# Performance work log

Hardware: AMD Instinct MI355X
Metric: run time of the kernel (lower is better)

Reference implementation:

```python
import jax, jax.numpy as jnp
import numpy as np

N, IN, WS, OUT, H = 50000, 256, 128, 32, 4
E, M, K = 800000, 2, 10
D = OUT * H  # 128
NEG_SLOPE = 0.2


def _decay(n, alpha=1.5):
    k = np.arange(1, n + 1)
    x = 1.0 / np.power(k, alpha)
    return (x / x.sum()).astype(np.float32)


def setup_inputs() -> dict:
    key = jax.random.key(0)
    ks = jax.random.split(key, 16)
    h = jax.random.normal(ks[0], (N, IN), dtype=jnp.float32)
    src0 = jax.random.randint(ks[1], (E,), 0, N, dtype=jnp.int32)
    dst0 = jax.random.randint(ks[2], (E,), 0, N, dtype=jnp.int32)
    src1 = jax.random.randint(ks[3], (E,), 0, N, dtype=jnp.int32)
    dst1 = jax.random.randint(ks[4], (E,), 0, N, dtype=jnp.int32)
    s = 0.05
    Wh = jax.random.normal(ks[5], (WS, IN), dtype=jnp.float32) * s
    # layer 0 (per metapath): fc (H*F, WS), attn_l/attn_r (H, F)
    fc0 = jax.random.normal(ks[6], (M, H * OUT, WS), dtype=jnp.float32) * s
    al0 = jax.random.normal(ks[7], (M, H, OUT), dtype=jnp.float32) * s
    ar0 = jax.random.normal(ks[8], (M, H, OUT), dtype=jnp.float32) * s
    # layer 1 (per metapath): fc (H*F, H*F)
    fc1 = jax.random.normal(ks[9], (M, H * OUT, H * OUT), dtype=jnp.float32) * s
    al1 = jax.random.normal(ks[10], (M, H, OUT), dtype=jnp.float32) * s
    ar1 = jax.random.normal(ks[11], (M, H, OUT), dtype=jnp.float32) * s
    Wp1 = jax.random.normal(ks[12], (128, D), dtype=jnp.float32) * s
    bp1 = jnp.zeros((128,), dtype=jnp.float32)
    Wp2 = jax.random.normal(ks[13], (1, 128), dtype=jnp.float32) * s
    return dict(h=h, src0=src0, dst0=dst0, src1=src1, dst1=dst1, Wh=Wh,
                fc0=fc0, al0=al0, ar0=ar0, fc1=fc1, al1=al1, ar1=ar1,
                Wp1=Wp1, bp1=bp1, Wp2=Wp2)


def gat_layer(x, src, dst, fcW, attn_l, attn_r):
    # x: (N, Din); fcW: (H*F, Din)
    ft = (x @ fcW.T).reshape(N, H, OUT)            # (N, H, F)
    el = jnp.sum(ft * attn_l, axis=-1)             # (N, H)
    er = jnp.sum(ft * attn_r, axis=-1)             # (N, H)
    e = jax.nn.leaky_relu(el[src] + er[dst], NEG_SLOPE)  # (E, H)
    # edge softmax over incoming edges of each destination node
    mx = jax.ops.segment_max(e, dst, num_segments=N)     # (N, H)
    ee = jnp.exp(e - mx[dst])
    sm = jax.ops.segment_sum(ee, dst, num_segments=N)    # (N, H)
    a = ee / sm[dst]                                     # (E, H)
    # global top-k over the edge dimension (th.topk dim=0), per head
    scores, idx = jax.lax.top_k(a.T, K)                  # (H, K)
    scores = jax.nn.softmax(scores, axis=-1)             # softmax over k
    a_new = jnp.zeros_like(a).at[idx, jnp.arange(H)[:, None]].set(scores)
    msg = ft[src] * a_new[:, :, None]                    # (E, H, F)
    out = jax.ops.segment_sum(msg, dst, num_segments=N)  # (N, H, F)
    return jax.nn.elu(out).reshape(N, H * OUT)


def reference(h, src0, dst0, src1, dst1, Wh, fc0, al0, ar0, fc1, al1, ar1, Wp1, bp1, Wp2):
    c = _decay(2, 1.5)
    wh = h @ Wh.T  # (N, WS)
    srcs = (src0, src1)
    dsts = (dst0, dst1)
    embs = []
    for i in range(M):
        a = gat_layer(wh, srcs[i], dsts[i], fc0[i], al0[i], ar0[i])  # (N, D)
        b = gat_layer(a, srcs[i], dsts[i], fc1[i], al1[i], ar1[i])   # (N, D)
        embs.append(a * c[0] + b * c[1])
    z = jnp.stack(embs, axis=1)                                      # (N, M, D)
    w = jnp.tanh(z @ Wp1.T + bp1) @ Wp2.T                            # (N, M, 1)
    beta = jax.nn.softmax(w, axis=1)
    return jnp.sum(beta * z, axis=1)                                 # (N, D)
```

## Files before the change

### kernel.cpp

```cpp
#include <hip/hip_runtime.h>
#include <math.h>

#define NN   50000
#define IN_F 256
#define OUTF 32
#define NH   4
#define NE   800000
#define NM   2
#define NK   10
#define ND   128

#define WROWS 32
#define WCK  32

#define NCB  782
#define CCAP 1280
#define DSH  6
#define DMSK 63
#define NSL  32
#define SLW  245

__device__ __forceinline__ float lrelu(float x){ return x >= 0.f ? x : 0.2f*x; }
__device__ __forceinline__ unsigned fmap(float f){
  unsigned u = __float_as_uint(f);
  return (u & 0x80000000u) ? ~u : (u | 0x80000000u);
}
__device__ __forceinline__ float funmap(unsigned u){
  return (u & 0x80000000u) ? __uint_as_float(u & 0x7FFFFFFFu) : __uint_as_float(~u);
}

__global__ __launch_bounds__(256) void k_plpr(
    const float* __restrict__ fc0, const float* __restrict__ al0, const float* __restrict__ ar0,
    const float* __restrict__ fc1, const float* __restrict__ al1, const float* __restrict__ ar1,
    float* __restrict__ plpr)
{
  int idx = blockIdx.x*256 + threadIdx.x;
  if (idx >= 4096) return;
  int w  = idx & 127;
  int hh = (idx >> 7) & 3;
  int lr = (idx >> 9) & 1;
  int m  = (idx >> 10) & 1;
  int L  = (idx >> 11) & 1;
  const float* fc = L ? fc1 : fc0;
  const float* at = L ? (lr ? ar1 : al1) : (lr ? ar0 : al0);
  float s = 0.f;
  for (int f = 0; f < OUTF; f++)
    s += at[(m*NH + hh)*OUTF + f] * fc[((size_t)m*128 + hh*OUTF + f)*128 + w];
  plpr[idx] = s;
}

__global__ __launch_bounds__(256) void k_wh(
    const float* __restrict__ hmat, const float* __restrict__ Whm,
    const float* __restrict__ plpr,
    float* __restrict__ wh, float* __restrict__ el0, float* __restrict__ er0)
{
  __shared__ float hsT[WCK][WROWS + 4];
  __shared__ float wT[WCK][128 + 4];
  __shared__ float PL[16][132];
  const int tid = threadIdx.x;
  const int r0 = blockIdx.x * WROWS;
  const int cgrp = tid & 31;
  const int rgrp = tid >> 5;
  float acc[4][4];
#pragma unroll
  for (int i = 0; i < 4; i++)
#pragma unroll
    for (int j = 0; j < 4; j++) acc[i][j] = 0.f;

  for (int kc = 0; kc < IN_F; kc += WCK){
    {
      int row = tid >> 3, f4 = tid & 7;
      int grow = r0 + row;
      float4 v = make_float4(0.f,0.f,0.f,0.f);
      if (grow < NN) v = *(const float4*)&hmat[(size_t)grow*IN_F + kc + f4*4];
      hsT[f4*4+0][row] = v.x;
      hsT[f4*4+1][row] = v.y;
      hsT[f4*4+2][row] = v.z;
      hsT[f4*4+3][row] = v.w;
    }
#pragma unroll
    for (int it = 0; it < 4; it++){
      int item = it*256 + tid;
      int col = item >> 3, f4 = item & 7;
      float4 v = *(const float4*)&Whm[(size_t)col*IN_F + kc + f4*4];
      wT[f4*4+0][col] = v.x;
      wT[f4*4+1][col] = v.y;
      wT[f4*4+2][col] = v.z;
      wT[f4*4+3][col] = v.w;
    }
    __syncthreads();
    for (int kk = 0; kk < WCK; kk++){
      float4 a = *(const float4*)&hsT[kk][rgrp*4];
      float4 b = *(const float4*)&wT[kk][cgrp*4];
      acc[0][0] += a.x*b.x; acc[0][1] += a.x*b.y; acc[0][2] += a.x*b.z; acc[0][3] += a.x*b.w;
      acc[1][0] += a.y*b.x; acc[1][1] += a.y*b.y; acc[1][2] += a.y*b.z; acc[1][3] += a.y*b.w;
      acc[2][0] += a.z*b.x; acc[2][1] += a.z*b.y; acc[2][2] += a.z*b.z; acc[2][3] += a.z*b.w;
      acc[3][0] += a.w*b.x; acc[3][1] += a.w*b.y; acc[3][2] += a.w*b.z; acc[3][3] += a.w*b.w;
    }
    __syncthreads();
  }
#pragma unroll
  for (int i = 0; i < 4; i++){
    int row = r0 + rgrp*4 + i;
    if (row < NN){
      float4 v = make_float4(acc[i][0], acc[i][1], acc[i][2], acc[i][3]);
      *(float4*)&wh[(size_t)row*ND + cgrp*4] = v;
    }
  }
#pragma unroll
  for (int i = 0; i < 4; i++)
    *(float4*)&wT[rgrp*4 + i][cgrp*4] = make_float4(acc[i][0], acc[i][1], acc[i][2], acc[i][3]);
  for (int i = tid; i < 16*128; i += 256) PL[i >> 7][i & 127] = plpr[i];
  __syncthreads();
  if (tid < 128){
    int r = tid >> 2, tcol = tid & 3;
    int row = r0 + r;
    if (row < NN){
      float a0 = 0.f, a1 = 0.f, a2 = 0.f, a3 = 0.f;
      const float* p0 = &PL[tcol*4+0][0];
      const float* p1 = &PL[tcol*4+1][0];
      const float* p2 = &PL[tcol*4+2][0];
      const float* p3 = &PL[tcol*4+3][0];
      for (int w4 = 0; w4 < 32; w4++){
        float4 v = *(const float4*)&wT[r][w4*4];
        const float4 q0 = *(const float4*)&p0[w4*4];
        const float4 q1 = *(const float4*)&p1[w4*4];
        const float4 q2 = *(const float4*)&p2[w4*4];
        const float4 q3 = *(const float4*)&p3[w4*4];
        a0 += v.x*q0.x; a0 += v.y*q0.y; a0 += v.z*q0.z; a0 += v.w*q0.w;
        a1 += v.x*q1.x; a1 += v.y*q1.y; a1 += v.z*q1.z; a1 += v.w*q1.w;
        a2 += v.x*q2.x; a2 += v.y*q2.y; a2 += v.z*q2.z; a2 += v.w*q2.w;
        a3 += v.x*q3.x; a3 += v.y*q3.y; a3 += v.z*q3.z; a3 += v.w*q3.w;
      }
      int m = tcol >> 1;
      float* dp = (tcol & 1) ? er0 : el0;
      float4 res = make_float4(a0, a1, a2, a3);
      *(float4*)&dp[((size_t)m*NN + row)*4] = res;
    }
  }
}

__global__ __launch_bounds__(256) void k_part(
    const int* __restrict__ s0, const int* __restrict__ d0,
    const int* __restrict__ s1, const int* __restrict__ d1,
    unsigned* __restrict__ ccnt, unsigned long long* __restrict__ coarse)
{
  int m = blockIdx.y;
  const int* sp = m ? s1 : s0;
  const int* dp = m ? d1 : d0;
  __shared__ unsigned hist[NCB], base[NCB], cur[NCB];
  int tid = threadIdx.x;
  for (int j = tid; j < NCB; j += 256){ hist[j] = 0u; cur[j] = 0u; }
  __syncthreads();
  int per = (NE + gridDim.x - 1) / gridDim.x;
  int e0 = blockIdx.x * per;
  int e1 = e0 + per; if (e1 > NE) e1 = NE;
  for (int i = e0 + tid; i < e1; i += 256)
    atomicAdd(&hist[dp[i] >> DSH], 1u);
  __syncthreads();
  for (int j = tid; j < NCB; j += 256)
    base[j] = hist[j] ? atomicAdd(&ccnt[m*NCB + j], hist[j]) : 0u;
  __syncthreads();
  for (int i = e0 + tid; i < e1; i += 256){
    int d = dp[i];
    int b = d >> DSH;
    unsigned loc = atomicAdd(&cur[b], 1u);
    unsigned pos = base[b] + loc;
    if (pos < CCAP)
      coarse[((size_t)m*NCB + b)*CCAP + pos] =
          ((unsigned long long)(unsigned)i << 24)
        | ((unsigned long long)(unsigned)(d & DMSK) << 16)
        | (unsigned long long)(unsigned)sp[i];
  }
}

__global__ __launch_bounds__(256) void k_fused(
    const unsigned* __restrict__ ccnt, const unsigned long long* __restrict__ coarse,
    const float* __restrict__ el, const float* __restrict__ er,
    unsigned long long* __restrict__ cand)
{
  int bb = blockIdx.x, m = blockIdx.y;
  const unsigned long long* ce = coarse + ((size_t)m*NCB + bb)*CCAP;
  unsigned cnt = ccnt[m*NCB + bb]; if (cnt > CCAP) cnt = CCAP;
  const float* elp = el + (size_t)m*NN*4;
  const float* erp = er + (size_t)m*NN*4;
  int tid = threadIdx.x;
  int h = tid & 3, es = tid >> 2;
  int dbase = bb << DSH;

  __shared__ float4 erL[64];
  __shared__ unsigned mxL[64][4];
  __shared__ unsigned long long smL[64][4];
  __shared__ unsigned metaL[CCAP];
  __shared__ unsigned long long smem_u64[CCAP*2];
  float* eL = (float*)smem_u64;
  unsigned long long (*cs)[NK] = (unsigned long long(*)[NK])smem_u64;

  if (tid < 64){
    int d = dbase + tid;
    erL[tid] = (d < NN) ? *(const float4*)&erp[(size_t)d*4] : make_float4(0.f,0.f,0.f,0.f);
  }
  { int j = tid; mxL[j>>2][j&3] = 0u; smL[j>>2][j&3] = 0ULL; }
  __syncthreads();

  {
    unsigned p = es;
    for (; p + 192 < cnt; p += 256){
      unsigned long long v0 = ce[p], v1 = ce[p+64], v2 = ce[p+128], v3 = ce[p+192];
      float g0 = elp[(unsigned)(v0 & 0xFFFFULL)*4 + h];
      float g1 = elp[(unsigned)(v1 & 0xFFFFULL)*4 + h];
      float g2 = elp[(unsigned)(v2 & 0xFFFFULL)*4 + h];
      float g3 = elp[(unsigned)(v3 & 0xFFFFULL)*4 + h];
      unsigned d0 = (unsigned)((v0 >> 16) & 0xFFULL);
      unsigned d1 = (unsigned)((v1 >> 16) & 0xFFULL);
      unsigned d2 = (unsigned)((v2 >> 16) & 0xFFULL);
      unsigned d3 = (unsigned)((v3 >> 16) & 0xFFULL);
      float e0 = lrelu(g0 + ((const float*)&erL[d0])[h]);
      float e1 = lrelu(g1 + ((const float*)&erL[d1])[h]);
      float e2 = lrelu(g2 + ((const float*)&erL[d2])[h]);
      float e3 = lrelu(g3 + ((const float*)&erL[d3])[h]);
      eL[p*4 + h] = e0; eL[(p+64)*4 + h] = e1;
      eL[(p+128)*4 + h] = e2; eL[(p+192)*4 + h] = e3;
      if (h == 0){
        metaL[p]     = ((unsigned)(v0 >> 24) << 8) | d0;
        metaL[p+64]  = ((unsigned)(v1 >> 24) << 8) | d1;
        metaL[p+128] = ((unsigned)(v2 >> 24) << 8) | d2;
        metaL[p+192] = ((unsigned)(v3 >> 24) << 8) | d3;
      }
      atomicMax(&mxL[d0][h], fmap(e0));
      atomicMax(&mxL[d1][h], fmap(e1));
      atomicMax(&mxL[d2][h], fmap(e2));
      atomicMax(&mxL[d3][h], fmap(e3));
    }
    for (; p < cnt; p += 64){
      unsigned long long v = ce[p];
      unsigned src  = (unsigned)(v & 0xFFFFULL);
      unsigned dloc = (unsigned)((v >> 16) & 0xFFULL);
      float e = lrelu(elp[src*4 + h] + ((const float*)&erL[dloc])[h]);
      eL[p*4 + h] = e;
      if (h == 0) metaL[p] = ((unsigned)(v >> 24) << 8) | dloc;
      atomicMax(&mxL[dloc][h], fmap(e));
    }
  }
  __syncthreads();

  for (unsigned p = es; p < cnt; p += 64){
    unsigned dloc = metaL[p] & 255u;
    float e = eL[p*4 + h];
    atomicAdd(&smL[dloc][h],
        (unsigned long long)llrint((double)expf(e - funmap(mxL[dloc][h])) * 1073741824.0));
  }
  __syncthreads();

  unsigned long long top[NK];
#pragma unroll
  for (int k = 0; k < NK; k++) top[k] = 0ULL;
  for (unsigned p = es; p < cnt; p += 64){
    unsigned mt = metaL[p];
    unsigned dloc = mt & 255u;
    unsigned eid  = mt >> 8;
    float e = eL[p*4 + h];
    float smv = (float)((double)smL[dloc][h] * (1.0/1073741824.0));
    float av = expf(e - funmap(mxL[dloc][h])) / smv;
    unsigned long long key = ((unsigned long long)__float_as_uint(av) << 32)
                           | (unsigned long long)(~eid);
    if (key > top[NK-1]){
#pragma unroll
      for (int k = 0; k < NK; k++){
        unsigned long long hi = key > top[k] ? key : top[k];
        unsigned long long lo = key > top[k] ? top[k] : key;
        top[k] = hi; key = lo;
      }
    }
  }
  __syncthreads();

  int row = h*64 + es;
#pragma unroll
  for (int k = 0; k < NK; k++) cs[row][k] = top[k];
  __syncthreads();
  int w = tid >> 6, lane = tid & 63;
  unsigned long long mytop[NK];
#pragma unroll
  for (int k = 0; k < NK; k++) mytop[k] = cs[w*64 + lane][k];
  unsigned long long best = 0ULL; int bp = -1;
#pragma unroll
  for (int k = 0; k < NK; k++) if (mytop[k] > best){ best = mytop[k]; bp = k; }
  for (int r = 0; r < NK; r++){
    unsigned long long b = best; int srcl = lane;
#pragma unroll
    for (int off = 32; off > 0; off >>= 1){
      unsigned long long ob = __shfl_down(b, off, 64);
      int os = __shfl_down(srcl, off, 64);
      if (ob > b){ b = ob; srcl = os; }
    }
    b = __shfl(b, 0, 64); srcl = __shfl(srcl, 0, 64);
    if (lane == 0) cand[(((size_t)m*NH + w)*NCB + blockIdx.x)*NK + r] = b;
    if (lane == srcl && bp >= 0){
#pragma unroll
      for (int k = 0; k < NK; k++) if (k == bp) mytop[k] = 0ULL;
      best = 0ULL; bp = -1;
#pragma unroll
      for (int k = 0; k < NK; k++) if (mytop[k] > best){ best = mytop[k]; bp = k; }
    }
  }
}

__global__ __launch_bounds__(256) void k_merge1(
    const unsigned long long* __restrict__ cand,
    unsigned long long* __restrict__ cand2)
{
  int hh = blockIdx.x, m = blockIdx.y, z = blockIdx.z;
  int tid = threadIdx.x;
  const unsigned long long* cp = cand + ((size_t)m*NH + hh)*((size_t)NCB*NK);
  int start = z*SLW;
  int end = start + SLW; if (end > NCB*NK) end = NCB*NK;
  unsigned long long mykey = (start + tid < end) ? cp[start + tid] : 0ULL;

  __shared__ unsigned long long red[256];
  __shared__ int redpos[256];
  for (int r = 0; r < NK; r++){
    red[tid] = mykey; redpos[tid] = tid;
    __syncthreads();
    for (int st = 128; st > 0; st >>= 1){
      if (tid < st && red[tid+st] > red[tid]){ red[tid] = red[tid+st]; redpos[tid] = redpos[tid+st]; }
      __syncthreads();
    }
    if (tid == 0)
      cand2[(((size_t)m*NH + hh)*NSL + z)*NK + r] = red[0];
    int winner = redpos[0];
    __syncthreads();
    if (tid == winner) mykey = 0ULL;
  }
}

__global__ __launch_bounds__(256) void k_sel(
    const unsigned long long* __restrict__ cand2,
    const int* __restrict__ s0, const int* __restrict__ d0,
    const int* __restrict__ s1, const int* __restrict__ d1,
    const float* __restrict__ ftsrc,
    const int* __restrict__ idsA,
    const float* __restrict__ fcW,
    const float* __restrict__ plpr1,
    int* __restrict__ idsOut, float* __restrict__ valsOut,
    float* __restrict__ el2, float* __restrict__ er2, int layer)
{
  int m = blockIdx.x;
  int tid = threadIdx.x;
  const int* sp = m ? s1 : s0;
  const int* dp = m ? d1 : d0;
  int wv = tid >> 6, lane = tid & 63;

  __shared__ unsigned long long selL[NH][NK];
  __shared__ float scL[NH][NK];
  __shared__ int snL[NH][NK], dL[NH][NK];
  __shared__ int slotOf[NH][NK], srcOf[NH][NK];

  {
    const unsigned long long* cp = cand2 + ((size_t)m*NH + wv)*((size_t)NSL*NK);
    unsigned long long top[NK];
#pragma unroll
    for (int k = 0; k < NK; k++) top[k] = 0ULL;
    for (int i = lane; i < NSL*NK; i += 64){
      unsigned long long key = cp[i];
      if (key > top[NK-1]){
#pragma unroll
        for (int k = 0; k < NK; k++){
          unsigned long long hi = key > top[k] ? key : top[k];
          unsigned long long lo = key > top[k] ? top[k] : key;
          top[k] = hi; key = lo;
        }
      }
    }
    unsigned long long best = 0ULL; int bp = -1;
#pragma unroll
    for (int k = 0; k < NK; k++) if (top[k] > best){ best = top[k]; bp = k; }
    for (int r = 0; r < NK; r++){
      unsigned long long b = best; int srcl = lane;
#pragma unroll
      for (int off = 32; off > 0; off >>= 1){
        unsigned long long ob = __shfl_down(b, off, 64);
        int os = __shfl_down(srcl, off, 64);
        if (ob > b){ b = ob; srcl = os; }
      }
      b = __shfl(b, 0, 64); srcl = __shfl(srcl, 0, 64);
      if (lane == 0) selL[wv][r] = b;
      if (lane == srcl && bp >= 0){
#pragma unroll
        for (int k = 0; k < NK; k++) if (k == bp) top[k] = 0ULL;
        best = 0ULL; bp = -1;
#pragma unroll
        for (int k = 0; k < NK; k++) if (top[k] > best){ best = top[k]; bp = k; }
      }
    }
  }
  __syncthreads();

  if (tid < NH*NK){
    int h = tid / NK, k = tid % NK;
    int e = (int)(~(unsigned)(selL[h][k] & 0xFFFFFFFFULL));
    snL[h][k] = sp[e];
    dL[h][k]  = dp[e];
  }
  __syncthreads();

  if (tid < NH){
    float v0 = __uint_as_float((unsigned)(selL[tid][0] >> 32));
    float p[NK]; float sum = 0.f;
#pragma unroll
    for (int k = 0; k < NK; k++){
      float v = __uint_as_float((unsigned)(selL[tid][k] >> 32));
      p[k] = expf(v - v0); sum += p[k];
    }
#pragma unroll
    for (int k = 0; k < NK; k++) scL[tid][k] = p[k] / sum;
  }

  if (wv == 0){
    int myA = -1;
    if (layer) myA = idsA[m*64 + lane];
    int myid = -1;
    int cnt = 0;
    for (int h = 0; h < NH; h++){
      for (int k = 0; k < NK; k++){
        int sn = snL[h][k], d = dL[h][k];
        int srcslot = sn;
        bool ok = true;
        if (layer){
          unsigned long long mb = __ballot(myA == sn);
          if (mb) srcslot = __ffsll(mb) - 1;
          else ok = false;
        }
        int slot = -1;
        if (ok){
          unsigned long long mm = __ballot(lane < cnt && myid == d);
          if (mm) slot = __ffsll(mm) - 1;
          else { slot = cnt; if (lane == cnt) myid = d; cnt++; }
        }
        if (lane == 0){ slotOf[h][k] = slot; srcOf[h][k] = srcslot; }
      }
    }
    idsOut[m*64 + lane] = (lane < cnt) ? myid : -1;
  }
  __syncthreads();

  float* vals = valsOut + (size_t)m*64*128;
  {
    int h = wv, f = lane;
    if (f < OUTF){
      const float* wr = fcW + ((size_t)m*128 + h*OUTF + f)*128;
      for (int k = 0; k < NK; k++){
        int slot = slotOf[h][k];
        if (slot < 0) continue;
        int srcS = srcOf[h][k];
        const float* x = layer ? (ftsrc + ((size_t)m*64 + srcS)*128)
                               : (ftsrc + (size_t)srcS*128);
        float dsum = 0.f;
        for (int w = 0; w < 128; w++) dsum += x[w] * wr[w];
        vals[(size_t)slot*128 + h*OUTF + f] += scL[h][k] * dsum;
      }
    }
  }
  __syncthreads();

  for (int t = tid; t < 64*128; t += 256){
    int slot = t >> 7, c = t & 127;
    float x = vals[(size_t)slot*128 + c];
    vals[(size_t)slot*128 + c] = x > 0.f ? x : expm1f(x);
  }
  __syncthreads();

  if (layer == 0){
    for (int t = tid; t < 64*8; t += 256){
      int slot = t >> 3, q = t & 7;
      int d = idsOut[m*64 + slot];
      if (d < 0) continue;
      int lr = q >> 2, hh = q & 3;
      const float* P = plpr1 + (((size_t)m*2 + lr)*NH + hh)*128;
      const float* row = vals + (size_t)slot*128;
      float s = 0.f;
      for (int w = 0; w < 128; w++) s += row[w] * P[w];
      float* dpp = lr ? er2 : el2;
      dpp[((size_t)m*NN + d)*4 + hh] = s;
    }
  }
}

__global__ __launch_bounds__(128) void k_final(
    const int* __restrict__ ids, const float* __restrict__ vals,
    const float* __restrict__ Wp1, const float* __restrict__ bp1, const float* __restrict__ Wp2,
    float c0, float c1, float* __restrict__ out)
{
  int j = blockIdx.x;
  int n = ids[j];
  if (n < 0) return;
  for (int q = 0; q < j; q++) if (ids[q] == n) return;
  int tid = threadIdx.x;
  __shared__ float z[2][128];
  __shared__ int slots[4];
  if (tid < 4){
    int sl = -1;
    const int* base = ids + tid*64;
    for (int q = 0; q < 64; q++) if (base[q] == n){ sl = q; break; }
    slots[tid] = sl;
  }
  __syncthreads();
#pragma unroll
  for (int m = 0; m < 2; m++){
    int sa = slots[m], sb = slots[2 + m];
    float av = sa >= 0 ? vals[((size_t)m*64 + sa)*128 + tid] : 0.f;
    float bv = sb >= 0 ? vals[((size_t)(2 + m)*64 + sb)*128 + tid] : 0.f;
    z[m][tid] = c0*av + c1*bv;
  }
  __syncthreads();
  float a0 = bp1[tid], a1 = a0;
  const float* wr = Wp1 + (size_t)tid*128;
  for (int w = 0; w < 128; w++){
    float wv = wr[w];
    a0 += z[0][w]*wv;
    a1 += z[1][w]*wv;
  }
  float t0 = tanhf(a0), t1 = tanhf(a1);
  float w2v = Wp2[tid];
  __shared__ float r0[128], r1[128];
  r0[tid] = t0*w2v; r1[tid] = t1*w2v;
  __syncthreads();
  for (int st = 64; st > 0; st >>= 1){
    if (tid < st){ r0[tid] += r0[tid+st]; r1[tid] += r1[tid+st]; }
    __syncthreads();
  }
  __shared__ float b0s, b1s;
  if (tid == 0){
    float w0 = r0[0], w1 = r1[0];
    float mxv = fmaxf(w0, w1);
    float e0 = expf(w0 - mxv), e1 = expf(w1 - mxv);
    float s = e0 + e1;
    b0s = e0/s; b1s = e1/s;
  }
  __syncthreads();
  out[(size_t)n*ND + tid] = b0s*z[0][tid] + b1s*z[1][tid];
}

extern "C" void kernel_launch(void* const* d_in, const int* in_sizes, int n_in,
                              void* d_out, int out_size, void* d_ws, size_t ws_size,
                              hipStream_t stream)
{
  const float* h    = (const float*)d_in[0];
  const int*   src0 = (const int*)d_in[1];
  const int*   dst0 = (const int*)d_in[2];
  const int*   src1 = (const int*)d_in[3];
  const int*   dst1 = (const int*)d_in[4];
  const float* Wh   = (const float*)d_in[5];
  const float* fc0  = (const float*)d_in[6];
  const float* al0  = (const float*)d_in[7];
  const float* ar0  = (const float*)d_in[8];
  const float* fc1  = (const float*)d_in[9];
  const float* al1  = (const float*)d_in[10];
  const float* ar1  = (const float*)d_in[11];
  const float* Wp1  = (const float*)d_in[12];
  const float* bp1  = (const float*)d_in[13];
  const float* Wp2  = (const float*)d_in[14];
  float* out = (float*)d_out;

  char* ws = (char*)d_ws;
  size_t off = 0;
  auto alloc = [&](size_t b){ size_t o = off; off = (off + b + 255) & ~(size_t)255; return o; };
  size_t o_el0    = alloc((size_t)NM*NN*4*4);
  size_t o_er0    = alloc((size_t)NM*NN*4*4);
  size_t o_plpr   = alloc(4096*4);
  size_t o_cand   = alloc((size_t)NM*NH*NCB*NK*8);
  size_t o_cand2  = alloc((size_t)NM*NH*NSL*NK*8);
  size_t o_coarse = alloc((size_t)NM*NCB*CCAP*8);
  size_t o_zs     = off;
  size_t o_ccnt   = alloc((size_t)NM*NCB*4);
  size_t o_el2    = alloc((size_t)NM*NN*4*4);
  size_t o_er2    = alloc((size_t)NM*NN*4*4);
  size_t o_vals   = alloc((size_t)2*NM*64*128*4);
  size_t zlen = off - o_zs;
  size_t o_ids    = alloc((size_t)2*NM*64*4);
  (void)ws_size; (void)in_sizes; (void)n_in;

  float* whp   = out;
  float* el0p  = (float*)(ws + o_el0);
  float* er0p  = (float*)(ws + o_er0);
  float* plprp = (float*)(ws + o_plpr);
  unsigned long long* candp  = (unsigned long long*)(ws + o_cand);
  unsigned long long* cand2p = (unsigned long long*)(ws + o_cand2);
  unsigned long long* coarsep = (unsigned long long*)(ws + o_coarse);
  unsigned* ccntp = (unsigned*)(ws + o_ccnt);
  float* el2p  = (float*)(ws + o_el2);
  float* er2p  = (float*)(ws + o_er2);
  float* valsp = (float*)(ws + o_vals);
  int*   idsp  = (int*)(ws + o_ids);
  float* vals0p = valsp;
  float* vals1p = valsp + (size_t)NM*64*128;
  int* ids0p = idsp;
  int* ids1p = idsp + NM*64;
  float* plpr1p = plprp + 2048;

  double x1 = 1.0 / (2.0 * sqrt(2.0));
  double ssum = 1.0 + x1;
  float c0 = (float)(1.0/ssum), c1 = (float)(x1/ssum);

  hipMemsetAsync(ws + o_zs, 0, zlen, stream);

  k_plpr<<<16, 256, 0, stream>>>(fc0, al0, ar0, fc1, al1, ar1, plprp);
  k_wh<<<(NN + WROWS - 1)/WROWS, 256, 0, stream>>>(h, Wh, plprp, whp, el0p, er0p);

  k_part<<<dim3(256, NM), 256, 0, stream>>>(src0, dst0, src1, dst1, ccntp, coarsep);

  dim3 gf(NCB, NM);
  dim3 gm1(NH, NM, NSL);

  k_fused<<<gf, 256, 0, stream>>>(ccntp, coarsep, el0p, er0p, candp);
  k_merge1<<<gm1, 256, 0, stream>>>(candp, cand2p);
  k_sel<<<NM, 256, 0, stream>>>(cand2p, src0, dst0, src1, dst1, whp,
                                (const int*)nullptr, fc0, plpr1p,
                                ids0p, vals0p, el2p, er2p, 0);
  hipMemsetAsync(d_out, 0, (size_t)out_size*sizeof(float), stream);

  k_fused<<<gf, 256, 0, stream>>>(ccntp, coarsep, el2p, er2p, candp);
  k_merge1<<<gm1, 256, 0, stream>>>(candp, cand2p);
  k_sel<<<NM, 256, 0, stream>>>(cand2p, src0, dst0, src1, dst1, vals0p,
                                ids0p, fc1, plpr1p,
                                ids1p, vals1p, el2p, er2p, 1);

  k_final<<<256, 128, 0, stream>>>(idsp, valsp, Wp1, bp1, Wp2, c0, c1, out);
}
```

Measured before the change: 348.8 us.

## Skip full wh projection; fold Wh into attention vectors and recompute selected rows

The full N×128 wh matrix is no longer computed. The attention projection vectors are premultiplied by Wh into a 16×256 matrix, so el/er come straight from h with a 16-column dot product per row instead of a 128-wide GEMM followed by a reduction. wh is then recomputed only for the few top-k source nodes inside the layer-0 selection kernel. This removes a large GEMM and the 25 MB write of wh, at the cost of more shared memory in k_sel and a different floating-point summation order.

```diff
diff --git a/kernel.cpp b/kernel.cpp
--- a/kernel.cpp
+++ b/kernel.cpp
@@ -9,9 +9,6 @@
 #define NM   2
 #define NK   10
 #define ND   128
-
-#define WROWS 32
-#define WCK  32
 
 #define NCB  782
 #define CCAP 1280
@@ -49,94 +46,63 @@
   plpr[idx] = s;
 }
 
-__global__ __launch_bounds__(256) void k_wh(
-    const float* __restrict__ hmat, const float* __restrict__ Whm,
-    const float* __restrict__ plpr,
-    float* __restrict__ wh, float* __restrict__ el0, float* __restrict__ er0)
-{
-  __shared__ float hsT[WCK][WROWS + 4];
-  __shared__ float wT[WCK][128 + 4];
-  __shared__ float PL[16][132];
-  const int tid = threadIdx.x;
-  const int r0 = blockIdx.x * WROWS;
-  const int cgrp = tid & 31;
-  const int rgrp = tid >> 5;
-  float acc[4][4];
-#pragma unroll
-  for (int i = 0; i < 4; i++)
-#pragma unroll
-    for (int j = 0; j < 4; j++) acc[i][j] = 0.f;
-
-  for (int kc = 0; kc < IN_F; kc += WCK){
-    {
-      int row = tid >> 3, f4 = tid & 7;
+__global__ __launch_bounds__(256) void k_p2(
+    const float* __restrict__ plpr, const float* __restrict__ Whm, float* __restrict__ P2)
+{
+  int idx = blockIdx.x*256 + threadIdx.x;
+  if (idx >= 16*256) return;
+  int q = idx >> 8, k = idx & 255;
+  float s = 0.f;
+  for (int w = 0; w < 128; w++)
+    s += plpr[q*128 + w] * Whm[(size_t)w*IN_F + k];
+  P2[q*256 + k] = s;
+}
+
+__global__ __launch_bounds__(256) void k_el(
+    const float* __restrict__ hmat, const float* __restrict__ P2,
+    float* __restrict__ el0, float* __restrict__ er0)
+{
+  __shared__ float hs[64][68];
+  __shared__ float PL2[16][260];
+  int tid = threadIdx.x;
+  int r0 = blockIdx.x * 64;
+  for (int i = tid; i < 16*64; i += 256){
+    int q = i >> 6, k4 = i & 63;
+    float4 v = ((const float4*)P2)[q*64 + k4];
+    *(float4*)&PL2[q][k4*4] = v;
+  }
+  int r = tid >> 2, c = tid & 3;
+  float a0 = 0.f, a1 = 0.f, a2 = 0.f, a3 = 0.f;
+  for (int kc = 0; kc < IN_F; kc += 64){
+#pragma unroll
+    for (int it = 0; it < 4; it++){
+      int item = it*256 + tid;
+      int row = item >> 4, f4 = item & 15;
       int grow = r0 + row;
       float4 v = make_float4(0.f,0.f,0.f,0.f);
-      if (grow < NN) v = *(const float4*)&hmat[(size_t)grow*IN_F + kc + f4*4];
-      hsT[f4*4+0][row] = v.x;
-      hsT[f4*4+1][row] = v.y;
-      hsT[f4*4+2][row] = v.z;
-      hsT[f4*4+3][row] = v.w;
-    }
-#pragma unroll
-    for (int it = 0; it < 4; it++){
-      int item = it*256 + tid;
-      int col = item >> 3, f4 = item & 7;
-      float4 v = *(const float4*)&Whm[(size_t)col*IN_F + kc + f4*4];
-      wT[f4*4+0][col] = v.x;
-      wT[f4*4+1][col] = v.y;
-      wT[f4*4+2][col] = v.z;
-      wT[f4*4+3][col] = v.w;
+      if (grow < NN) v = ((const float4*)hmat)[(size_t)grow*64 + (kc >> 2) + f4];
+      *(float4*)&hs[row][f4*4] = v;
     }
     __syncthreads();
-    for (int kk = 0; kk < WCK; kk++){
-      float4 a = *(const float4*)&hsT[kk][rgrp*4];
-      float4 b = *(const float4*)&wT[kk][cgrp*4];
-      acc[0][0] += a.x*b.x; acc[0][1] += a.x*b.y; acc[0][2] += a.x*b.z; acc[0][3] += a.x*b.w;
-      acc[1][0] += a.y*b.x; acc[1][1] += a.y*b.y; acc[1][2] += a.y*b.z; acc[1][3] += a.y*b.w;
-      acc[2][0] += a.z*b.x; acc[2][1] += a.z*b.y; acc[2][2] += a.z*b.z; acc[2][3] += a.z*b.w;
-      acc[3][0] += a.w*b.x; acc[3][1] += a.w*b.y; acc[3][2] += a.w*b.z; acc[3][3] += a.w*b.w;
+#pragma unroll
+    for (int k4 = 0; k4 < 16; k4++){
+      float4 hv = *(const float4*)&hs[r][k4*4];
+      float4 u0 = *(const float4*)&PL2[c*4+0][kc + k4*4];
+      float4 u1 = *(const float4*)&PL2[c*4+1][kc + k4*4];
+      float4 u2 = *(const float4*)&PL2[c*4+2][kc + k4*4];
+      float4 u3 = *(const float4*)&PL2[c*4+3][kc + k4*4];
+      a0 += hv.x*u0.x; a0 += hv.y*u0.y; a0 += hv.z*u0.z; a0 += hv.w*u0.w;
+      a1 += hv.x*u1.x; a1 += hv.y*u1.y; a1 += hv.z*u1.z; a1 += hv.w*u1.w;
+      a2 += hv.x*u2.x; a2 += hv.y*u2.y; a2 += hv.z*u2.z; a2 += hv.w*u2.w;
+      a3 += hv.x*u3.x; a3 += hv.y*u3.y; a3 += hv.z*u3.z; a3 += hv.w*u3.w;
     }
     __syncthreads();
   }
-#pragma unroll
-  for (int i = 0; i < 4; i++){
-    int row = r0 + rgrp*4 + i;
-    if (row < NN){
-      float4 v = make_float4(acc[i][0], acc[i][1], acc[i][2], acc[i][3]);
-      *(float4*)&wh[(size_t)row*ND + cgrp*4] = v;
-    }
-  }
-#pragma unroll
-  for (int i = 0; i < 4; i++)
-    *(float4*)&wT[rgrp*4 + i][cgrp*4] = make_float4(acc[i][0], acc[i][1], acc[i][2], acc[i][3]);
-  for (int i = tid; i < 16*128; i += 256) PL[i >> 7][i & 127] = plpr[i];
-  __syncthreads();
-  if (tid < 128){
-    int r = tid >> 2, tcol = tid & 3;
-    int row = r0 + r;
-    if (row < NN){
-      float a0 = 0.f, a1 = 0.f, a2 = 0.f, a3 = 0.f;
-      const float* p0 = &PL[tcol*4+0][0];
-      const float* p1 = &PL[tcol*4+1][0];
-      const float* p2 = &PL[tcol*4+2][0];
-      const float* p3 = &PL[tcol*4+3][0];
-      for (int w4 = 0; w4 < 32; w4++){
-        float4 v = *(const float4*)&wT[r][w4*4];
-        const float4 q0 = *(const float4*)&p0[w4*4];
-        const float4 q1 = *(const float4*)&p1[w4*4];
-        const float4 q2 = *(const float4*)&p2[w4*4];
-        const float4 q3 = *(const float4*)&p3[w4*4];
-        a0 += v.x*q0.x; a0 += v.y*q0.y; a0 += v.z*q0.z; a0 += v.w*q0.w;
-        a1 += v.x*q1.x; a1 += v.y*q1.y; a1 += v.z*q1.z; a1 += v.w*q1.w;
-        a2 += v.x*q2.x; a2 += v.y*q2.y; a2 += v.z*q2.z; a2 += v.w*q2.w;
-        a3 += v.x*q3.x; a3 += v.y*q3.y; a3 += v.z*q3.z; a3 += v.w*q3.w;
-      }
-      int m = tcol >> 1;
-      float* dp = (tcol & 1) ? er0 : el0;
-      float4 res = make_float4(a0, a1, a2, a3);
-      *(float4*)&dp[((size_t)m*NN + row)*4] = res;
-    }
+  int row = r0 + r;
+  if (row < NN){
+    int m = c >> 1;
+    float* dp = (c & 1) ? er0 : el0;
+    *(float4*)&dp[((size_t)m*NN + row)*4] = make_float4(a0, a1, a2, a3);
   }
 }
 
@@ -338,6 +304,7 @@
     const unsigned long long* __restrict__ cand2,
     const int* __restrict__ s0, const int* __restrict__ d0,
     const int* __restrict__ s1, const int* __restrict__ d1,
+    const float* __restrict__ hmat, const float* __restrict__ Whm,
     const float* __restrict__ ftsrc,
     const int* __restrict__ idsA,
     const float* __restrict__ fcW,
@@ -355,6 +322,8 @@
   __shared__ float scL[NH][NK];
   __shared__ int snL[NH][NK], dL[NH][NK];
   __shared__ int slotOf[NH][NK], srcOf[NH][NK];
+  __shared__ float whL[NH*NK][132];
+  __shared__ float hsrc[NH*NK][260];
 
   {
     const unsigned long long* cp = cand2 + ((size_t)m*NH + wv)*((size_t)NSL*NK);
@@ -444,6 +413,33 @@
   }
   __syncthreads();
 
+  if (layer == 0){
+    for (int t = tid; t < NH*NK*64; t += 256){
+      int e = t >> 6, k4 = t & 63;
+      int src = (&snL[0][0])[e];
+      float4 v = ((const float4*)hmat)[(size_t)src*64 + k4];
+      *(float4*)&hsrc[e][k4*4] = v;
+    }
+    __syncthreads();
+    int w = tid & 127, half = tid >> 7;
+    float acc2[20];
+#pragma unroll
+    for (int i = 0; i < 20; i++) acc2[i] = 0.f;
+    const float4* wp = (const float4*)&Whm[(size_t)w*IN_F];
+    for (int k4 = 0; k4 < 64; k4++){
+      float4 wv2 = wp[k4];
+#pragma unroll
+      for (int i = 0; i < 20; i++){
+        float4 hv = *(const float4*)&hsrc[half + 2*i][k4*4];
+        acc2[i] += hv.x*wv2.x; acc2[i] += hv.y*wv2.y;
+        acc2[i] += hv.z*wv2.z; acc2[i] += hv.w*wv2.w;
+      }
+    }
+#pragma unroll
+    for (int i = 0; i < 20; i++) whL[half + 2*i][w] = acc2[i];
+    __syncthreads();
+  }
+
   float* vals = valsOut + (size_t)m*64*128;
   {
     int h = wv, f = lane;
@@ -452,9 +448,8 @@
       for (int k = 0; k < NK; k++){
         int slot = slotOf[h][k];
         if (slot < 0) continue;
-        int srcS = srcOf[h][k];
-        const float* x = layer ? (ftsrc + ((size_t)m*64 + srcS)*128)
-                               : (ftsrc + (size_t)srcS*128);
+        const float* x = layer ? (ftsrc + ((size_t)m*64 + srcOf[h][k])*128)
+                               : &whL[h*NK + k][0];
         float dsum = 0.f;
         for (int w = 0; w < 128; w++) dsum += x[w] * wr[w];
         vals[(size_t)slot*128 + h*OUTF + f] += scL[h][k] * dsum;
@@ -568,6 +563,7 @@
   size_t o_el0    = alloc((size_t)NM*NN*4*4);
   size_t o_er0    = alloc((size_t)NM*NN*4*4);
   size_t o_plpr   = alloc(4096*4);
+  size_t o_p2     = alloc(16*256*4);
   size_t o_cand   = alloc((size_t)NM*NH*NCB*NK*8);
   size_t o_cand2  = alloc((size_t)NM*NH*NSL*NK*8);
   size_t o_coarse = alloc((size_t)NM*NCB*CCAP*8);
@@ -580,10 +576,10 @@
   size_t o_ids    = alloc((size_t)2*NM*64*4);
   (void)ws_size; (void)in_sizes; (void)n_in;
 
-  float* whp   = out;
   float* el0p  = (float*)(ws + o_el0);
   float* er0p  = (float*)(ws + o_er0);
   float* plprp = (float*)(ws + o_plpr);
+  float* p2p   = (float*)(ws + o_p2);
   unsigned long long* candp  = (unsigned long long*)(ws + o_cand);
   unsigned long long* cand2p = (unsigned long long*)(ws + o_cand2);
   unsigned long long* coarsep = (unsigned long long*)(ws + o_coarse);
@@ -602,10 +598,12 @@
   double ssum = 1.0 + x1;
   float c0 = (float)(1.0/ssum), c1 = (float)(x1/ssum);
 
+  hipMemsetAsync(d_out, 0, (size_t)out_size*sizeof(float), stream);
   hipMemsetAsync(ws + o_zs, 0, zlen, stream);
 
   k_plpr<<<16, 256, 0, stream>>>(fc0, al0, ar0, fc1, al1, ar1, plprp);
-  k_wh<<<(NN + WROWS - 1)/WROWS, 256, 0, stream>>>(h, Wh, plprp, whp, el0p, er0p);
+  k_p2<<<16, 256, 0, stream>>>(plprp, Wh, p2p);
+  k_el<<<(NN + 63)/64, 256, 0, stream>>>(h, p2p, el0p, er0p);
 
   k_part<<<dim3(256, NM), 256, 0, stream>>>(src0, dst0, src1, dst1, ccntp, coarsep);
 
@@ -614,15 +612,14 @@
 
   k_fused<<<gf, 256, 0, stream>>>(ccntp, coarsep, el0p, er0p, candp);
   k_merge1<<<gm1, 256, 0, stream>>>(candp, cand2p);
-  k_sel<<<NM, 256, 0, stream>>>(cand2p, src0, dst0, src1, dst1, whp,
-                                (const int*)nullptr, fc0, plpr1p,
+  k_sel<<<NM, 256, 0, stream>>>(cand2p, src0, dst0, src1, dst1, h, Wh,
+                                (const float*)nullptr, (const int*)nullptr, fc0, plpr1p,
                                 ids0p, vals0p, el2p, er2p, 0);
-  hipMemsetAsync(d_out, 0, (size_t)out_size*sizeof(float), stream);
 
   k_fused<<<gf, 256, 0, stream>>>(ccntp, coarsep, el2p, er2p, candp);
   k_merge1<<<gm1, 256, 0, stream>>>(candp, cand2p);
-  k_sel<<<NM, 256, 0, stream>>>(cand2p, src0, dst0, src1, dst1, vals0p,
-                                ids0p, fc1, plpr1p,
+  k_sel<<<NM, 256, 0, stream>>>(cand2p, src0, dst0, src1, dst1, h, Wh,
+                                vals0p, ids0p, fc1, plpr1p,
                                 ids1p, vals1p, el2p, er2p, 1);
 
   k_final<<<256, 128, 0, stream>>>(idsp, valsp, Wp1, bp1, Wp2, c0, c1, out);
```

Measured after the change: 341.5 us. 1.02x faster.
